# Kernel optimization log

Hardware: AMD Instinct MI355X
Metric: run time of the kernel (lower is better)

Reference implementation:

```python
import jax, jax.numpy as jnp
import numpy as np

D_MODEL = 768
N_HEADS = 12
D_K = D_MODEL // N_HEADS
SCALE = 1.0 / np.sqrt(D_K).astype(np.float32)


def setup_inputs() -> dict:
    key = jax.random.key(0)
    ks = jax.random.split(key, 11)
    B, S, D = 2, 2048, D_MODEL
    std = 1.0 / np.sqrt(D).astype(np.float32)
    x = jax.random.normal(ks[0], (B, S, D), dtype=jnp.float32)
    def lin(kw, kb):
        W = jax.random.normal(kw, (D, D), dtype=jnp.float32) * std
        b = jax.random.normal(kb, (D,), dtype=jnp.float32) * std
        return W, b
    Wq, bq = lin(ks[1], ks[2])
    Wk, bk = lin(ks[3], ks[4])
    Wv, bv = lin(ks[5], ks[6])
    Wo, bo = lin(ks[7], ks[8])   # linear_w_out
    Wf, bf = lin(ks[9], ks[10])  # linear_final_layer
    return {"x": x, "Wq": Wq, "bq": bq, "Wk": Wk, "bk": bk, "Wv": Wv,
            "bv": bv, "Wo": Wo, "bo": bo, "Wf": Wf, "bf": bf}


def reference(x, Wq, bq, Wk, bk, Wv, bv, Wo, bo, Wf, bf):
    B, S, D = x.shape
    H, dk = N_HEADS, D_K
    # torch Linear: y = x @ W.T + b
    q = (x @ Wq.T + bq).reshape(B, H, S, dk)  # faithful: view, NOT transpose-split
    k = (x @ Wk.T + bk).reshape(B, H, S, dk)
    v = (x @ Wv.T + bv).reshape(B, H, S, dk)
    # scores = q @ k^T  -> [B,H,S,S]
    scores = jnp.einsum('bhsd,bhtd->bhst', q, k)
    # faithful quirk: softmax AFTER (scores/sqrt(dk)) @ v, over d_k axis
    attn = jax.nn.softmax(jnp.einsum('bhst,bhtd->bhsd', scores * SCALE, v), axis=-1)
    multi_head = attn.reshape(B, S, D)
    multi_head = multi_head @ Wo.T + bo
    out = multi_head @ Wf.T + bf
    return out
```

## Files before the change

kernel.cpp:

```cpp
#include <hip/hip_runtime.h>
#include <math.h>

typedef unsigned short u16;
typedef unsigned int   u32;
typedef __attribute__((ext_vector_type(8))) _Float16 f16x8;
typedef __attribute__((ext_vector_type(4))) float f32x4;

#define DMODEL 768
#define SEQ    2048
#define BATCH  2
#define NHEAD  12
#define DKH    64
#define PER_BATCH (SEQ*DMODEL)
#define PER_HEAD  (SEQ*DKH)
#define ATT_SCALE 0.125f

__device__ inline u16 f2h(float f) {
    _Float16 h = (_Float16)f;
    return *(u16*)&h;
}

__device__ inline void async_load16(const void* g, void* l) {
    __builtin_amdgcn_global_load_lds(
        (const __attribute__((address_space(1))) unsigned int*)g,
        (__attribute__((address_space(3))) unsigned int*)l, 16, 0, 0);
}

__global__ void conv_all(const float* __restrict__ x,
                         const float* __restrict__ Wq, const float* __restrict__ Wk,
                         const float* __restrict__ Wv, const float* __restrict__ Wf,
                         const float* __restrict__ Wo,
                         const float* __restrict__ bo, const float* __restrict__ bfb,
                         u16* xh, u16* Wh3, u16* Wfh, u16* WoT, float* bc)
{
    const int z = blockIdx.y;
    if (z == 5) {
        if (blockIdx.x >= 48) return;
        const int row    = blockIdx.x * 16 + (threadIdx.x >> 4);
        const int lane16 = threadIdx.x & 15;
        const float* r = Wf + (size_t)row * 768;
        float s = 0.f;
        #pragma unroll
        for (int t = 0; t < 48; ++t) s += r[lane16 + 16 * t] * bo[lane16 + 16 * t];
        #pragma unroll
        for (int off = 8; off > 0; off >>= 1) s += __shfl_xor(s, off, 64);
        if (lane16 == 0) bc[row] = s + bfb[row];
        return;
    }
    if (z == 6) {
        __shared__ u16 S[32][33];
        const int bi = blockIdx.x / 24, bj = blockIdx.x % 24;
        const int r  = threadIdx.x >> 3;
        const int c4 = threadIdx.x & 7;
        float4 v = *(const float4*)&Wo[(size_t)(bi * 32 + r) * 768 + bj * 32 + c4 * 4];
        S[c4 * 4 + 0][r] = f2h(v.x); S[c4 * 4 + 1][r] = f2h(v.y);
        S[c4 * 4 + 2][r] = f2h(v.z); S[c4 * 4 + 3][r] = f2h(v.w);
        __syncthreads();
        u16 o0 = S[r][c4 * 4 + 0], o1 = S[r][c4 * 4 + 1];
        u16 o2 = S[r][c4 * 4 + 2], o3 = S[r][c4 * 4 + 3];
        uint2 pk; pk.x = (u32)o0 | ((u32)o1 << 16); pk.y = (u32)o2 | ((u32)o3 << 16);
        *(uint2*)&WoT[(size_t)(bj * 32 + r) * 768 + bi * 32 + c4 * 4] = pk;
        return;
    }
    const float* src; u16* dst; int n;
    switch (z) {
        case 0: src = x;  dst = xh;            n = 3145728; break;
        case 1: src = Wq; dst = Wh3;           n = 589824;  break;
        case 2: src = Wk; dst = Wh3 + 589824;  n = 589824;  break;
        case 3: src = Wv; dst = Wh3 + 1179648; n = 589824;  break;
        default:src = Wf; dst = Wfh;           n = 589824;  break;
    }
    const int n4 = n >> 2;
    for (int i = blockIdx.x * blockDim.x + threadIdx.x; i < n4; i += gridDim.x * blockDim.x) {
        float4 v = ((const float4*)src)[i];
        u16 h0 = f2h(v.x), h1 = f2h(v.y), h2 = f2h(v.z), h3 = f2h(v.w);
        uint2 hp; hp.x = (u32)h0 | ((u32)h1 << 16); hp.y = (u32)h2 | ((u32)h3 << 16);
        ((uint2*)dst)[i] = hp;
    }
}

__global__ __launch_bounds__(256, 3) void qkv_gemm(
    const u16* __restrict__ Ah, const u16* __restrict__ Wh,
    const float* __restrict__ b0, const float* __restrict__ b1, const float* __restrict__ b2,
    float* __restrict__ C0, float* __restrict__ C1, float* __restrict__ C2)
{
    const int tid = threadIdx.x;
    const int w   = tid >> 6;
    const int L   = tid & 63;
    const int wr  = w >> 1, wc = w & 1;
    const int mBase = blockIdx.x * 128;
    const int nBase = blockIdx.y * 128;
    const int sel  = nBase / 768;
    const int nOff = nBase % 768;

    __shared__ __align__(16) u16 As[128 * 64];
    __shared__ __align__(16) u16 Bs[128 * 64];

    f32x4 acc[4][4];
    #pragma unroll
    for (int i = 0; i < 4; ++i)
        #pragma unroll
        for (int j = 0; j < 4; ++j)
            acc[i][j] = (f32x4){0.f, 0.f, 0.f, 0.f};

    const int srow = L >> 3;
    const int kScr = ((L & 7) ^ (srow & 7)) * 8;
    const int rin = L & 15, q = L >> 4;

    for (int kb = 0; kb < 768; kb += 64) {
        if (kb) __syncthreads();
        #pragma unroll
        for (int cc = 0; cc < 2; ++cc) {
            const int ch = w * 2 + cc;
            const size_t rA = (size_t)(mBase + ch * 16 + srow) * 768 + kb + kScr;
            async_load16(&Ah[rA],           &As[ch * 1024]);
            async_load16(&Ah[rA + 8 * 768], &As[ch * 1024 + 512]);
            const size_t rB = (size_t)(nBase + ch * 16 + srow) * 768 + kb + kScr;
            async_load16(&Wh[rB],           &Bs[ch * 1024]);
            async_load16(&Wh[rB + 8 * 768], &Bs[ch * 1024 + 512]);
        }
        __syncthreads();

        #pragma unroll
        for (int kq = 0; kq < 2; ++kq) {
            const int slot = ((kq * 4 + q) ^ (rin & 7)) * 8;
            f16x8 af[4], bfr[4];
            #pragma unroll
            for (int i = 0; i < 4; ++i)
                af[i] = *(const f16x8*)&As[(wr * 64 + i * 16 + rin) * 64 + slot];
            #pragma unroll
            for (int j = 0; j < 4; ++j)
                bfr[j] = *(const f16x8*)&Bs[(wc * 64 + j * 16 + rin) * 64 + slot];
            #pragma unroll
            for (int i = 0; i < 4; ++i)
                #pragma unroll
                for (int j = 0; j < 4; ++j)
                    acc[i][j] = __builtin_amdgcn_mfma_f32_16x16x32_f16(af[i], bfr[j], acc[i][j], 0, 0, 0);
        }
    }

    const float* bsel = (sel == 0) ? b0 : ((sel == 1) ? b1 : b2);
    float* Csel = (sel == 0) ? C0 : ((sel == 1) ? C1 : C2);

    #pragma unroll
    for (int j = 0; j < 4; ++j) {
        const int c = nOff + wc * 64 + j * 16 + rin;
        const float bv = bsel[c];
        #pragma unroll
        for (int i = 0; i < 4; ++i) {
            const int r0 = mBase + wr * 64 + i * 16 + q * 4;
            #pragma unroll
            for (int reg = 0; reg < 4; ++reg)
                Csel[(size_t)(r0 + reg) * 768 + c] = acc[i][j][reg] + bv;
        }
    }
}

__global__ __launch_bounds__(256, 4) void gemm_f16(
    const u16* __restrict__ A, const u16* __restrict__ B,
    const float* __restrict__ bias, void* __restrict__ C, int out_f16)
{
    const int tid = threadIdx.x;
    const int w   = tid >> 6;
    const int L   = tid & 63;
    const int wr  = w >> 1, wc = w & 1;
    const int mBase = blockIdx.x * 64;
    const int nBase = blockIdx.y * 128;

    __shared__ __align__(16) u16 As[64 * 64];
    __shared__ __align__(16) u16 Bs[128 * 64];

    f32x4 acc[2][4];
    #pragma unroll
    for (int i = 0; i < 2; ++i)
        #pragma unroll
        for (int j = 0; j < 4; ++j)
            acc[i][j] = (f32x4){0.f, 0.f, 0.f, 0.f};

    const int srow = L >> 3;
    const int kScr = ((L & 7) ^ (srow & 7)) * 8;
    const int rin = L & 15, q = L >> 4;

    for (int kb = 0; kb < 768; kb += 64) {
        if (kb) __syncthreads();
        {
            const size_t rA = (size_t)(mBase + w * 16 + srow) * 768 + kb + kScr;
            async_load16(&A[rA],           &As[w * 1024]);
            async_load16(&A[rA + 8 * 768], &As[w * 1024 + 512]);
        }
        #pragma unroll
        for (int cc = 0; cc < 2; ++cc) {
            const int cB = w * 2 + cc;
            const size_t rB = (size_t)(nBase + cB * 16 + srow) * 768 + kb + kScr;
            async_load16(&B[rB],           &Bs[cB * 1024]);
            async_load16(&B[rB + 8 * 768], &Bs[cB * 1024 + 512]);
        }
        __syncthreads();

        #pragma unroll
        for (int kq = 0; kq < 2; ++kq) {
            const int slot = ((kq * 4 + q) ^ (rin & 7)) * 8;
            f16x8 af[2], bfr[4];
            #pragma unroll
            for (int i = 0; i < 2; ++i)
                af[i] = *(const f16x8*)&As[(wr * 2 + i) * 1024 + rin * 64 + slot];
            #pragma unroll
            for (int j = 0; j < 4; ++j)
                bfr[j] = *(const f16x8*)&Bs[(wc * 4 + j) * 1024 + rin * 64 + slot];
            #pragma unroll
            for (int i = 0; i < 2; ++i)
                #pragma unroll
                for (int j = 0; j < 4; ++j)
                    acc[i][j] = __builtin_amdgcn_mfma_f32_16x16x32_f16(af[i], bfr[j], acc[i][j], 0, 0, 0);
        }
    }

    #pragma unroll
    for (int j = 0; j < 4; ++j) {
        const int c = nBase + wc * 64 + j * 16 + rin;
        const float bv = bias ? bias[c] : 0.f;
        #pragma unroll
        for (int i = 0; i < 2; ++i) {
            const int r0 = mBase + wr * 32 + i * 16 + q * 4;
            #pragma unroll
            for (int reg = 0; reg < 4; ++reg) {
                const float v = acc[i][j][reg] + bv;
                if (out_f16) ((u16*)C)[(size_t)(r0 + reg) * 768 + c] = f2h(v);
                else         ((float*)C)[(size_t)(r0 + reg) * 768 + c] = v;
            }
        }
    }
}

__global__ __launch_bounds__(256, 1) void kv_outer(
    const float* __restrict__ Kbuf, const float* __restrict__ Vbuf,
    float* __restrict__ Mpart)
{
    const int chunk = blockIdx.x;
    const int p     = blockIdx.y;
    const int b = p / NHEAD, h = p % NHEAD;
    const float* Kb = Kbuf + (size_t)b * PER_BATCH + (size_t)h * PER_HEAD + (size_t)chunk * 128 * DKH;
    const float* Vb = Vbuf + (size_t)b * PER_BATCH + (size_t)h * PER_HEAD + (size_t)chunk * 128 * DKH;

    __shared__ __align__(16) float Ks[32][64];
    __shared__ __align__(16) float Vs[32][64];

    const int tid = threadIdx.x;
    const int tx  = tid & 15;
    const int ty  = tid >> 4;

    float acc[4][4];
    #pragma unroll
    for (int i = 0; i < 4; ++i)
        #pragma unroll
        for (int j = 0; j < 4; ++j) acc[i][j] = 0.f;

    for (int t0 = 0; t0 < 128; t0 += 32) {
        #pragma unroll
        for (int r = 0; r < 2; ++r) {
            int idx = tid + 256 * r;
            int row = idx >> 4;
            int c4  = idx & 15;
            *(float4*)&Ks[row][c4 * 4] = *(const float4*)&Kb[(size_t)(t0 + row) * DKH + c4 * 4];
            *(float4*)&Vs[row][c4 * 4] = *(const float4*)&Vb[(size_t)(t0 + row) * DKH + c4 * 4];
        }
        __syncthreads();
        #pragma unroll
        for (int tt = 0; tt < 32; ++tt) {
            float4 ka = *(const float4*)&Ks[tt][ty * 4];
            float4 va = *(const float4*)&Vs[tt][tx * 4];
            float a[4] = {ka.x, ka.y, ka.z, ka.w};
            float v[4] = {va.x, va.y, va.z, va.w};
            #pragma unroll
            for (int i = 0; i < 4; ++i)
                #pragma unroll
                for (int j = 0; j < 4; ++j)
                    acc[i][j] += a[i] * v[j];
        }
        __syncthreads();
    }

    float* Mo = Mpart + ((size_t)p * 16 + chunk) * 4096;
    #pragma unroll
    for (int i = 0; i < 4; ++i)
        #pragma unroll
        for (int j = 0; j < 4; ++j)
            Mo[(ty * 4 + i) * 64 + tx * 4 + j] = acc[i][j];
}

__global__ __launch_bounds__(256, 2) void reduce_M(
    const float* __restrict__ Mpart, float* __restrict__ Mred)
{
    const int p = blockIdx.x;
    const int e4 = blockIdx.y * 256 + threadIdx.x;
    const float4* Mp4 = (const float4*)Mpart + (size_t)p * 16384;
    float4 s = Mp4[e4];
    #pragma unroll
    for (int c = 1; c < 16; ++c) {
        float4 t = Mp4[(size_t)c * 1024 + e4];
        s.x += t.x; s.y += t.y; s.z += t.z; s.w += t.w;
    }
    s.x *= ATT_SCALE; s.y *= ATT_SCALE; s.z *= ATT_SCALE; s.w *= ATT_SCALE;
    ((float4*)Mred)[(size_t)p * 1024 + e4] = s;
}

__global__ __launch_bounds__(256, 2) void attn_gemm(
    const float* __restrict__ Qbuf, const float* __restrict__ Mred,
    u16* __restrict__ MH)
{
    const int chunk = blockIdx.x;
    const int p     = blockIdx.y;
    const int b = p / NHEAD, h = p % NHEAD;
    const float* Qb = Qbuf + (size_t)b * PER_BATCH + (size_t)h * PER_HEAD + (size_t)chunk * 64 * DKH;
    u16* MHb        = MH   + (size_t)b * PER_BATCH + (size_t)h * PER_HEAD + (size_t)chunk * 64 * DKH;

    __shared__ float QsT[64][65];
    __shared__ __align__(16) float SM[64][64];

    const int tid = threadIdx.x;

    const float4* M4 = (const float4*)(Mred + (size_t)p * 4096);
    float4* SM4 = (float4*)SM;
    #pragma unroll
    for (int r = 0; r < 4; ++r) {
        int e4 = tid + 256 * r;
        SM4[e4] = M4[e4];
        int row = e4 >> 4, c4 = e4 & 15;
        float4 v = *(const float4*)&Qb[(size_t)row * DKH + c4 * 4];
        QsT[c4 * 4 + 0][row] = v.x; QsT[c4 * 4 + 1][row] = v.y;
        QsT[c4 * 4 + 2][row] = v.z; QsT[c4 * 4 + 3][row] = v.w;
    }
    __syncthreads();

    const int tx = tid & 15;
    const int ty = tid >> 4;

    float acc[4][4];
    #pragma unroll
    for (int i = 0; i < 4; ++i)
        #pragma unroll
        for (int j = 0; j < 4; ++j) acc[i][j] = 0.f;

    #pragma unroll 4
    for (int k = 0; k < 64; ++k) {
        float4 bv = *(const float4*)&SM[k][tx * 4];
        float aa[4] = {QsT[k][ty * 4 + 0], QsT[k][ty * 4 + 1],
                       QsT[k][ty * 4 + 2], QsT[k][ty * 4 + 3]};
        float bb[4] = {bv.x, bv.y, bv.z, bv.w};
        #pragma unroll
        for (int i = 0; i < 4; ++i)
            #pragma unroll
            for (int j = 0; j < 4; ++j)
                acc[i][j] += aa[i] * bb[j];
    }

    #pragma unroll
    for (int i = 0; i < 4; ++i) {
        float m = fmaxf(fmaxf(acc[i][0], acc[i][1]), fmaxf(acc[i][2], acc[i][3]));
        #pragma unroll
        for (int off = 1; off < 16; off <<= 1)
            m = fmaxf(m, __shfl_xor(m, off, 64));
        float e0 = __expf(acc[i][0] - m), e1 = __expf(acc[i][1] - m);
        float e2 = __expf(acc[i][2] - m), e3 = __expf(acc[i][3] - m);
        float s = (e0 + e1) + (e2 + e3);
        #pragma unroll
        for (int off = 1; off < 16; off <<= 1)
            s += __shfl_xor(s, off, 64);
        float inv = 1.f / s;
        u16 o0 = f2h(e0 * inv), o1 = f2h(e1 * inv);
        u16 o2 = f2h(e2 * inv), o3 = f2h(e3 * inv);
        uint2 pk; pk.x = (u32)o0 | ((u32)o1 << 16); pk.y = (u32)o2 | ((u32)o3 << 16);
        const int row = ty * 4 + i;
        *(uint2*)&MHb[(size_t)row * DKH + tx * 4] = pk;
    }
}

extern "C" void kernel_launch(void* const* d_in, const int* in_sizes, int n_in,
                              void* d_out, int out_size, void* d_ws, size_t ws_size,
                              hipStream_t stream)
{
    const float* x  = (const float*)d_in[0];
    const float* Wq = (const float*)d_in[1];
    const float* bq = (const float*)d_in[2];
    const float* Wk = (const float*)d_in[3];
    const float* bk = (const float*)d_in[4];
    const float* Wv = (const float*)d_in[5];
    const float* bv = (const float*)d_in[6];
    const float* Wo = (const float*)d_in[7];
    const float* bo = (const float*)d_in[8];
    const float* Wf = (const float*)d_in[9];
    const float* bf = (const float*)d_in[10];
    float* out = (float*)d_out;

    float* ws_f = (float*)d_ws;
    float* Q   = ws_f;
    float* Kb  = ws_f + 3145728;
    float* Vb  = ws_f + 6291456;
    float* Mp  = ws_f + 9437184;
    float* Mrd = ws_f + 11010048;
    float* bc  = ws_f + 11108352;
    u16* ub  = (u16*)(ws_f + 11109376);
    u16* xh  = ub;
    u16* Wh3 = ub + 3145728;
    u16* Wfh = Wh3 + 1769472;
    u16* WoT = Wfh + 589824;
    u16* Wcb = WoT + 589824;
    u16* MH  = xh;

    dim3 blk(256);
    conv_all<<<dim3(576, 7), blk, 0, stream>>>(x, Wq, Wk, Wv, Wf, Wo, bo, bf,
                                               xh, Wh3, Wfh, WoT, bc);
    qkv_gemm<<<dim3(32, 18), blk, 0, stream>>>(xh, Wh3, bq, bk, bv, Q, Kb, Vb);
    kv_outer<<<dim3(16, 24), blk, 0, stream>>>(Kb, Vb, Mp);
    reduce_M<<<dim3(24, 4), blk, 0, stream>>>(Mp, Mrd);
    gemm_f16<<<dim3(12, 6), blk, 0, stream>>>(Wfh, WoT, nullptr, Wcb, 1);
    attn_gemm<<<dim3(32, 24), blk, 0, stream>>>(Q, Mrd, MH);
    gemm_f16<<<dim3(64, 6), blk, 0, stream>>>(MH, Wcb, bc, out, 0);
}
```

Baseline: 159.6 us.

## Fold Wf·Wo GEMM into QKV launch, store K/V as fp16, atomically reduce KV outer products

The Wf×Wo combined-weight GEMM moves into the QKV GEMM launch as an extra grid row, which removes one kernel launch. K and V are now written as fp16 rather than fp32, cutting their write and read traffic. The separate partial-sum reduce kernel is gone: kv_outer accumulates scaled results into a zeroed Mred with atomicAdd, and conv_all gains a slice that does the zeroing. The costs are atomic contention, fp16 precision on K/V, and non-deterministic summation order.

Result: slower. 167.9 us (+5.2%).

```diff
diff --git a/kernel.cpp b/kernel.cpp
--- a/kernel.cpp
+++ b/kernel.cpp
@@ -19,6 +19,10 @@
     _Float16 h = (_Float16)f;
     return *(u16*)&h;
 }
+__device__ inline float4 h4f(uint2 v) {
+    _Float16* p = (_Float16*)&v;
+    return make_float4((float)p[0], (float)p[1], (float)p[2], (float)p[3]);
+}
 
 __device__ inline void async_load16(const void* g, void* l) {
     __builtin_amdgcn_global_load_lds(
@@ -31,7 +35,8 @@
                          const float* __restrict__ Wv, const float* __restrict__ Wf,
                          const float* __restrict__ Wo,
                          const float* __restrict__ bo, const float* __restrict__ bfb,
-                         u16* xh, u16* Wh3, u16* Wfh, u16* WoT, float* bc)
+                         u16* xh, u16* Wh3, u16* Wfh, u16* WoT, float* bc,
+                         float* Mred)
 {
     const int z = blockIdx.y;
     if (z == 5) {
@@ -50,6 +55,7 @@
     if (z == 6) {
         __shared__ u16 S[32][33];
         const int bi = blockIdx.x / 24, bj = blockIdx.x % 24;
+        if (blockIdx.x >= 576) return;
         const int r  = threadIdx.x >> 3;
         const int c4 = threadIdx.x & 7;
         float4 v = *(const float4*)&Wo[(size_t)(bi * 32 + r) * 768 + bj * 32 + c4 * 4];
@@ -62,6 +68,12 @@
         *(uint2*)&WoT[(size_t)(bj * 32 + r) * 768 + bi * 32 + c4 * 4] = pk;
         return;
     }
+    if (z == 7) {
+        if (blockIdx.x >= 96) return;
+        ((float4*)Mred)[(size_t)blockIdx.x * 256 + threadIdx.x] =
+            (float4){0.f, 0.f, 0.f, 0.f};
+        return;
+    }
     const float* src; u16* dst; int n;
     switch (z) {
         case 0: src = x;  dst = xh;            n = 3145728; break;
@@ -80,18 +92,32 @@
 }
 
 __global__ __launch_bounds__(256, 3) void qkv_gemm(
-    const u16* __restrict__ Ah, const u16* __restrict__ Wh,
-    const float* __restrict__ b0, const float* __restrict__ b1, const float* __restrict__ b2,
-    float* __restrict__ C0, float* __restrict__ C1, float* __restrict__ C2)
+    const u16* __restrict__ xh, const u16* __restrict__ Wh3,
+    const u16* __restrict__ Wfh, const u16* __restrict__ WoT,
+    const float* __restrict__ bq, const float* __restrict__ bk, const float* __restrict__ bv,
+    float* __restrict__ Q, u16* __restrict__ Kh, u16* __restrict__ Vh,
+    u16* __restrict__ Wcb)
 {
     const int tid = threadIdx.x;
     const int w   = tid >> 6;
     const int L   = tid & 63;
     const int wr  = w >> 1, wc = w & 1;
-    const int mBase = blockIdx.x * 128;
-    const int nBase = blockIdx.y * 128;
-    const int sel  = nBase / 768;
-    const int nOff = nBase % 768;
+
+    const u16 *Ap, *Bp;
+    int mBase, nBaseB, mode;
+    if (blockIdx.y == 18) {
+        if (blockIdx.x >= 36) return;
+        Ap = Wfh; Bp = WoT;
+        mBase  = (blockIdx.x / 6) * 128;
+        nBaseB = (blockIdx.x % 6) * 128;
+        mode = 3;
+    } else {
+        if (blockIdx.x >= 32) return;
+        Ap = xh; Bp = Wh3;
+        mBase  = blockIdx.x * 128;
+        nBaseB = blockIdx.y * 128;
+        mode = nBaseB / 768;
+    }
 
     __shared__ __align__(16) u16 As[128 * 64];
     __shared__ __align__(16) u16 Bs[128 * 64];
@@ -113,11 +139,11 @@
         for (int cc = 0; cc < 2; ++cc) {
             const int ch = w * 2 + cc;
             const size_t rA = (size_t)(mBase + ch * 16 + srow) * 768 + kb + kScr;
-            async_load16(&Ah[rA],           &As[ch * 1024]);
-            async_load16(&Ah[rA + 8 * 768], &As[ch * 1024 + 512]);
-            const size_t rB = (size_t)(nBase + ch * 16 + srow) * 768 + kb + kScr;
-            async_load16(&Wh[rB],           &Bs[ch * 1024]);
-            async_load16(&Wh[rB + 8 * 768], &Bs[ch * 1024 + 512]);
+            async_load16(&Ap[rA],           &As[ch * 1024]);
+            async_load16(&Ap[rA + 8 * 768], &As[ch * 1024 + 512]);
+            const size_t rB = (size_t)(nBaseB + ch * 16 + srow) * 768 + kb + kScr;
+            async_load16(&Bp[rB],           &Bs[ch * 1024]);
+            async_load16(&Bp[rB + 8 * 768], &Bs[ch * 1024 + 512]);
         }
         __syncthreads();
 
@@ -139,26 +165,30 @@
         }
     }
 
-    const float* bsel = (sel == 0) ? b0 : ((sel == 1) ? b1 : b2);
-    float* Csel = (sel == 0) ? C0 : ((sel == 1) ? C1 : C2);
+    const int nOff = (mode == 3) ? nBaseB : (nBaseB % 768);
+    const float* bias = (mode == 0) ? bq : ((mode == 1) ? bk : ((mode == 2) ? bv : nullptr));
+    u16* Ch = (mode == 1) ? Kh : ((mode == 2) ? Vh : Wcb);
 
     #pragma unroll
     for (int j = 0; j < 4; ++j) {
         const int c = nOff + wc * 64 + j * 16 + rin;
-        const float bv = bsel[c];
+        const float bvl = bias ? bias[c] : 0.f;
         #pragma unroll
         for (int i = 0; i < 4; ++i) {
             const int r0 = mBase + wr * 64 + i * 16 + q * 4;
             #pragma unroll
-            for (int reg = 0; reg < 4; ++reg)
-                Csel[(size_t)(r0 + reg) * 768 + c] = acc[i][j][reg] + bv;
+            for (int reg = 0; reg < 4; ++reg) {
+                const float v = acc[i][j][reg] + bvl;
+                if (mode == 0) Q[(size_t)(r0 + reg) * 768 + c] = v;
+                else           Ch[(size_t)(r0 + reg) * 768 + c] = f2h(v);
+            }
         }
     }
 }
 
 __global__ __launch_bounds__(256, 4) void gemm_f16(
     const u16* __restrict__ A, const u16* __restrict__ B,
-    const float* __restrict__ bias, void* __restrict__ C, int out_f16)
+    const float* __restrict__ bias, float* __restrict__ C)
 {
     const int tid = threadIdx.x;
     const int w   = tid >> 6;
@@ -218,29 +248,26 @@
     #pragma unroll
     for (int j = 0; j < 4; ++j) {
         const int c = nBase + wc * 64 + j * 16 + rin;
-        const float bv = bias ? bias[c] : 0.f;
+        const float bvl = bias[c];
         #pragma unroll
         for (int i = 0; i < 2; ++i) {
             const int r0 = mBase + wr * 32 + i * 16 + q * 4;
             #pragma unroll
-            for (int reg = 0; reg < 4; ++reg) {
-                const float v = acc[i][j][reg] + bv;
-                if (out_f16) ((u16*)C)[(size_t)(r0 + reg) * 768 + c] = f2h(v);
-                else         ((float*)C)[(size_t)(r0 + reg) * 768 + c] = v;
-            }
-        }
-    }
-}
-
-__global__ __launch_bounds__(256, 1) void kv_outer(
-    const float* __restrict__ Kbuf, const float* __restrict__ Vbuf,
-    float* __restrict__ Mpart)
+            for (int reg = 0; reg < 4; ++reg)
+                C[(size_t)(r0 + reg) * 768 + c] = acc[i][j][reg] + bvl;
+        }
+    }
+}
+
+__global__ __launch_bounds__(256, 2) void kv_outer(
+    const u16* __restrict__ Kh, const u16* __restrict__ Vh,
+    float* __restrict__ Mred)
 {
     const int chunk = blockIdx.x;
     const int p     = blockIdx.y;
     const int b = p / NHEAD, h = p % NHEAD;
-    const float* Kb = Kbuf + (size_t)b * PER_BATCH + (size_t)h * PER_HEAD + (size_t)chunk * 128 * DKH;
-    const float* Vb = Vbuf + (size_t)b * PER_BATCH + (size_t)h * PER_HEAD + (size_t)chunk * 128 * DKH;
+    const u16* Kb = Kh + (size_t)b * PER_BATCH + (size_t)h * PER_HEAD + (size_t)chunk * 128 * DKH;
+    const u16* Vb = Vh + (size_t)b * PER_BATCH + (size_t)h * PER_HEAD + (size_t)chunk * 128 * DKH;
 
     __shared__ __align__(16) float Ks[32][64];
     __shared__ __align__(16) float Vs[32][64];
@@ -256,13 +283,16 @@
         for (int j = 0; j < 4; ++j) acc[i][j] = 0.f;
 
     for (int t0 = 0; t0 < 128; t0 += 32) {
+        if (t0) __syncthreads();
         #pragma unroll
         for (int r = 0; r < 2; ++r) {
             int idx = tid + 256 * r;
             int row = idx >> 4;
             int c4  = idx & 15;
-            *(float4*)&Ks[row][c4 * 4] = *(const float4*)&Kb[(size_t)(t0 + row) * DKH + c4 * 4];
-            *(float4*)&Vs[row][c4 * 4] = *(const float4*)&Vb[(size_t)(t0 + row) * DKH + c4 * 4];
+            uint2 kp = *(const uint2*)&Kb[(size_t)(t0 + row) * DKH + c4 * 4];
+            uint2 vp = *(const uint2*)&Vb[(size_t)(t0 + row) * DKH + c4 * 4];
+            *(float4*)&Ks[row][c4 * 4] = h4f(kp);
+            *(float4*)&Vs[row][c4 * 4] = h4f(vp);
         }
         __syncthreads();
         #pragma unroll
@@ -277,31 +307,14 @@
                 for (int j = 0; j < 4; ++j)
                     acc[i][j] += a[i] * v[j];
         }
-        __syncthreads();
-    }
-
-    float* Mo = Mpart + ((size_t)p * 16 + chunk) * 4096;
+    }
+
+    float* Mo = Mred + (size_t)p * 4096;
     #pragma unroll
     for (int i = 0; i < 4; ++i)
         #pragma unroll
         for (int j = 0; j < 4; ++j)
-            Mo[(ty * 4 + i) * 64 + tx * 4 + j] = acc[i][j];
-}
-
-__global__ __launch_bounds__(256, 2) void reduce_M(
-    const float* __restrict__ Mpart, float* __restrict__ Mred)
-{
-    const int p = blockIdx.x;
-    const int e4 = blockIdx.y * 256 + threadIdx.x;
-    const float4* Mp4 = (const float4*)Mpart + (size_t)p * 16384;
-    float4 s = Mp4[e4];
-    #pragma unroll
-    for (int c = 1; c < 16; ++c) {
-        float4 t = Mp4[(size_t)c * 1024 + e4];
-        s.x += t.x; s.y += t.y; s.z += t.z; s.w += t.w;
-    }
-    s.x *= ATT_SCALE; s.y *= ATT_SCALE; s.z *= ATT_SCALE; s.w *= ATT_SCALE;
-    ((float4*)Mred)[(size_t)p * 1024 + e4] = s;
+            atomicAdd(&Mo[(ty * 4 + i) * 64 + tx * 4 + j], acc[i][j] * ATT_SCALE);
 }
 
 __global__ __launch_bounds__(256, 2) void attn_gemm(
@@ -394,26 +407,24 @@
 
     float* ws_f = (float*)d_ws;
     float* Q   = ws_f;
-    float* Kb  = ws_f + 3145728;
-    float* Vb  = ws_f + 6291456;
-    float* Mp  = ws_f + 9437184;
-    float* Mrd = ws_f + 11010048;
-    float* bc  = ws_f + 11108352;
-    u16* ub  = (u16*)(ws_f + 11109376);
+    float* Mrd = ws_f + 3145728;
+    float* bc  = ws_f + 3244032;
+    u16* ub  = (u16*)(ws_f + 3245056);
     u16* xh  = ub;
     u16* Wh3 = ub + 3145728;
     u16* Wfh = Wh3 + 1769472;
     u16* WoT = Wfh + 589824;
     u16* Wcb = WoT + 589824;
+    u16* Kh  = Wcb + 589824;
+    u16* Vh  = Kh  + 3145728;
     u16* MH  = xh;
 
     dim3 blk(256);
-    conv_all<<<dim3(576, 7), blk, 0, stream>>>(x, Wq, Wk, Wv, Wf, Wo, bo, bf,
-                                               xh, Wh3, Wfh, WoT, bc);
-    qkv_gemm<<<dim3(32, 18), blk, 0, stream>>>(xh, Wh3, bq, bk, bv, Q, Kb, Vb);
-    kv_outer<<<dim3(16, 24), blk, 0, stream>>>(Kb, Vb, Mp);
-    reduce_M<<<dim3(24, 4), blk, 0, stream>>>(Mp, Mrd);
-    gemm_f16<<<dim3(12, 6), blk, 0, stream>>>(Wfh, WoT, nullptr, Wcb, 1);
+    conv_all<<<dim3(576, 8), blk, 0, stream>>>(x, Wq, Wk, Wv, Wf, Wo, bo, bf,
+                                               xh, Wh3, Wfh, WoT, bc, Mrd);
+    qkv_gemm<<<dim3(36, 19), blk, 0, stream>>>(xh, Wh3, Wfh, WoT, bq, bk, bv,
+                                               Q, Kh, Vh, Wcb);
+    kv_outer<<<dim3(16, 24), blk, 0, stream>>>(Kh, Vh, Mrd);
     attn_gemm<<<dim3(32, 24), blk, 0, stream>>>(Q, Mrd, MH);
-    gemm_f16<<<dim3(64, 6), blk, 0, stream>>>(MH, Wcb, bc, out, 0);
-}
+    gemm_f16<<<dim3(64, 6), blk, 0, stream>>>(MH, Wcb, bc, out);
+}
```
